# Optimization experiments

Measured on AMD Instinct MI355X. Metric: run time of the kernel, lower is better.

## Reference

```python
import jax, jax.numpy as jnp
import numpy as np

# Static diagonal offsets of the SparseDIA matrix (eqx static field).
OFFSETS = (-128, -64, -8, -1, 0, 1, 8, 64, 128)
N = 8192   # matrix dimension (diags.shape[1])
M = 4096   # number of dense columns in `other`


def setup_inputs() -> dict:
    key = jax.random.key(0)
    k1, k2 = jax.random.split(key)
    diags = jax.random.normal(k1, (len(OFFSETS), N), dtype=jnp.float32)
    other = jax.random.normal(k2, (N, M), dtype=jnp.float32)
    return {"diags": diags, "other": other}


def reference(diags, other):
    """SparseDIA._matmul_dense(left_matmul=True): out = A_dia @ other.

    For each static offset k, rows [top:bottom] of the output accumulate
    diag[start:end] (the valid part of the stored diagonal) times the
    matching rows of `other`. Offsets are Python ints, so all slices are
    static and jit-compatible.
    """
    n = other.shape[0]
    out = jnp.zeros_like(other)
    for k, offset in enumerate(OFFSETS):
        start = max(0, offset)
        end = min(n, n + offset)
        top = max(0, -offset)
        bottom = top + (end - start)
        out = out.at[top:bottom, :].add(
            diags[k, start:end, None] * other[start:end, :]
        )
    return out
```

## Files before the change

### kernel.cpp

```cpp
#include <hip/hip_runtime.h>


#define DIA_N   8192
#define DIA_M   4096
#define M4      (DIA_M / 4)
#define CB      8
#define BR      128
#define HALO    128
#define RING    512
#define NB      16
#define GROUP   (BR * NB)
#define THREADS 1024
#define NWAVES  (THREADS / 64)

typedef float f4 __attribute__((ext_vector_type(4)));
typedef __attribute__((address_space(3))) unsigned int       lds_uint;
typedef const __attribute__((address_space(1))) unsigned int glb_uint;

__global__ __launch_bounds__(THREADS, 8) void sparse_dia_kernel(
    const float* __restrict__ diags,
    const float* __restrict__ other,
    float* __restrict__ out)
{
    constexpr int OFF[9] = {-128, -64, -8, -1, 0, 1, 8, 64, 128};

    __shared__ f4    ring[RING][CB];
    __shared__ float dlds[2][9 * BR];

    const int tid  = threadIdx.x;
    const int gr0  = blockIdx.y * GROUP;
    const int cb4  = blockIdx.x * CB;

    const int wave = tid >> 6;
    const int lane = tid & 63;
    const int lrow = lane >> 3;
    const int lcol = lane & 7;
    const int scol = lcol ^ lrow;

    auto stage_ring = [&](int slot0, int q0, int ninst) {
#pragma unroll
        for (int s = 0; s < 3; ++s) {
            if (s >= ninst) break;
            const int inst = wave * ninst + s;
            int q = q0 + inst * 8 + lrow;
            q = (q < 0) ? 0 : (q >= DIA_N ? DIA_N - 1 : q);
            const float* src = other + ((size_t)q * DIA_M + (size_t)(cb4 + scol) * 4);
            __builtin_amdgcn_global_load_lds(
                (glb_uint*)src,
                (lds_uint*)&ring[slot0 + inst * 8][0],
                16, 0, 0);
        }
    };

    auto stage_diag = [&](int buf, int t) {
        const int bs = gr0 + t * BR;
        for (int f = tid; f < 9 * BR; f += THREADS) {
            const int k  = f >> 7;
            const int i  = f & (BR - 1);
            const int q  = bs + i + OFF[k];
            const int qc = (q < 0) ? 0 : (q >= DIA_N ? DIA_N - 1 : q);
            float v = diags[k * DIA_N + qc];
            v = ((unsigned)q < (unsigned)DIA_N) ? v : 0.f;
            dlds[buf][f] = v;
        }
    };

    f4* __restrict__ out4 = (f4*)out;

    stage_ring(0, gr0 - HALO, 3);
    stage_diag(0, 0);
    __syncthreads();

    const int c = tid & 7;
    const int i = tid >> 3;

    for (int t = 0; t < NB; ++t) {
        if (t + 1 < NB) {
            const int u = (BR + 2 * HALO) + t * BR;
            stage_ring(u & (RING - 1), gr0 - HALO + u, 1);
            stage_diag((t + 1) & 1, t + 1);
        }

        const int buf  = t & 1;
        const int base = (HALO + t * BR) & (RING - 1);

        float dk[9];
#pragma unroll
        for (int k = 0; k < 9; ++k) dk[k] = dlds[buf][k * BR + i];

        f4 a = (f4){0.f, 0.f, 0.f, 0.f};
#pragma unroll
        for (int k = 0; k < 9; ++k) {
            const int slot = (base + i + OFF[k]) & (RING - 1);
            a += dk[k] * ring[slot][c ^ (slot & 7)];
        }

        out4[(size_t)(gr0 + t * BR + i) * M4 + cb4 + c] = a;

        __syncthreads();
    }
}

extern "C" void kernel_launch(void* const* d_in, const int* in_sizes, int n_in,
                              void* d_out, int out_size, void* d_ws, size_t ws_size,
                              hipStream_t stream) {
    const float* diags = (const float*)d_in[0];
    const float* other = (const float*)d_in[1];
    float* out         = (float*)d_out;

    dim3 block(THREADS, 1, 1);
    dim3 grid(M4 / CB, DIA_N / GROUP, 1);
    sparse_dia_kernel<<<grid, block, 0, stream>>>(diags, other, out);
}
```

Baseline: 244.4 us.

## Pipeline ring staging with manual vmcnt waits and register-prefetched diagonals

Halves the block to 512 threads with 64-row tiles. Diagonal coefficients are now loaded straight from global memory into registers two tiles ahead, replacing the shared-memory double buffer. Each step uses explicit s_waitcnt vmcnt counts and raw s_barrier instead of __syncthreads, so the async LDS loads for later tiles stay in flight while the current tile is computed and stored. This relies on exact counts of outstanding vector-memory ops, which is fragile, and the smaller tiles double the number of barrier steps.

```diff
diff --git a/kernel.cpp b/kernel.cpp
--- a/kernel.cpp
+++ b/kernel.cpp
@@ -5,27 +5,25 @@
 #define DIA_M   4096
 #define M4      (DIA_M / 4)
 #define CB      8
-#define BR      128
+#define BR      64
 #define HALO    128
 #define RING    512
-#define NB      16
+#define NB      32
 #define GROUP   (BR * NB)
-#define THREADS 1024
-#define NWAVES  (THREADS / 64)
+#define THREADS 512
 
 typedef float f4 __attribute__((ext_vector_type(4)));
 typedef __attribute__((address_space(3))) unsigned int       lds_uint;
 typedef const __attribute__((address_space(1))) unsigned int glb_uint;
 
-__global__ __launch_bounds__(THREADS, 8) void sparse_dia_kernel(
+__global__ __launch_bounds__(THREADS, 4) void sparse_dia_kernel(
     const float* __restrict__ diags,
     const float* __restrict__ other,
     float* __restrict__ out)
 {
     constexpr int OFF[9] = {-128, -64, -8, -1, 0, 1, 8, 64, 128};
 
-    __shared__ f4    ring[RING][CB];
-    __shared__ float dlds[2][9 * BR];
+    __shared__ f4 ring[RING][CB];
 
     const int tid  = threadIdx.x;
     const int gr0  = blockIdx.y * GROUP;
@@ -37,68 +35,81 @@
     const int lcol = lane & 7;
     const int scol = lcol ^ lrow;
 
-    auto stage_ring = [&](int slot0, int q0, int ninst) {
+    const int c = tid & 7;
+    const int i = tid >> 3;
+
+    f4* __restrict__ out4 = (f4*)out;
+
+    auto gll8 = [&](int slot0, int q0) {
+        int q = q0 + lrow;
+        q = (q < 0) ? 0 : (q >= DIA_N ? DIA_N - 1 : q);
+        const float* src = other + ((size_t)q * DIA_M + (size_t)(cb4 + scol) * 4);
+        __builtin_amdgcn_global_load_lds((glb_uint*)src,
+            (lds_uint*)&ring[slot0][0], 16, 0, 0);
+    };
+
+    auto load_diag = [&](int t, float (&dk)[9]) {
+        const int b = gr0 + t * BR + i;
+        if (gr0 + t * BR - HALO >= 0 && gr0 + t * BR + (BR - 1) + HALO < DIA_N) {
 #pragma unroll
-        for (int s = 0; s < 3; ++s) {
-            if (s >= ninst) break;
-            const int inst = wave * ninst + s;
-            int q = q0 + inst * 8 + lrow;
-            q = (q < 0) ? 0 : (q >= DIA_N ? DIA_N - 1 : q);
-            const float* src = other + ((size_t)q * DIA_M + (size_t)(cb4 + scol) * 4);
-            __builtin_amdgcn_global_load_lds(
-                (glb_uint*)src,
-                (lds_uint*)&ring[slot0 + inst * 8][0],
-                16, 0, 0);
+            for (int k = 0; k < 9; ++k)
+                dk[k] = diags[k * DIA_N + b + OFF[k]];
+        } else {
+#pragma unroll
+            for (int k = 0; k < 9; ++k) {
+                const int q  = b + OFF[k];
+                const int qc = (q < 0) ? 0 : (q >= DIA_N ? DIA_N - 1 : q);
+                const float v = diags[k * DIA_N + qc];
+                dk[k] = ((unsigned)q < (unsigned)DIA_N) ? v : 0.f;
+            }
         }
     };
 
-    auto stage_diag = [&](int buf, int t) {
-        const int bs = gr0 + t * BR;
-        for (int f = tid; f < 9 * BR; f += THREADS) {
-            const int k  = f >> 7;
-            const int i  = f & (BR - 1);
-            const int q  = bs + i + OFF[k];
-            const int qc = (q < 0) ? 0 : (q >= DIA_N ? DIA_N - 1 : q);
-            float v = diags[k * DIA_N + qc];
-            v = ((unsigned)q < (unsigned)DIA_N) ? v : 0.f;
-            dlds[buf][f] = v;
-        }
-    };
-
-    f4* __restrict__ out4 = (f4*)out;
-
-    stage_ring(0, gr0 - HALO, 3);
-    stage_diag(0, 0);
-    __syncthreads();
-
-    const int c = tid & 7;
-    const int i = tid >> 3;
-
-    for (int t = 0; t < NB; ++t) {
-        if (t + 1 < NB) {
-            const int u = (BR + 2 * HALO) + t * BR;
-            stage_ring(u & (RING - 1), gr0 - HALO + u, 1);
-            stage_diag((t + 1) & 1, t + 1);
-        }
-
-        const int buf  = t & 1;
-        const int base = (HALO + t * BR) & (RING - 1);
-
-        float dk[9];
-#pragma unroll
-        for (int k = 0; k < 9; ++k) dk[k] = dlds[buf][k * BR + i];
-
+    auto compute_store = [&](int t, const float (&dk)[9]) {
+        const int L0 = t * BR + HALO + i;
         f4 a = (f4){0.f, 0.f, 0.f, 0.f};
 #pragma unroll
         for (int k = 0; k < 9; ++k) {
-            const int slot = (base + i + OFF[k]) & (RING - 1);
-            a += dk[k] * ring[slot][c ^ (slot & 7)];
+            const int s = (L0 + OFF[k]) & (RING - 1);
+            a += dk[k] * ring[s][c ^ (s & 7)];
         }
+        out4[(size_t)(gr0 + t * BR + i) * M4 + cb4 + c] = a;
+    };
 
-        out4[(size_t)(gr0 + t * BR + i) * M4 + cb4 + c] = a;
+    float dkA[9], dkB[9];
 
-        __syncthreads();
+#pragma unroll
+    for (int s = 0; s < 5; ++s) {
+        const int inst = wave * 5 + s;
+        gll8(inst * 8, gr0 - HALO + inst * 8);
     }
+    gll8(320 + wave * 8, gr0 - HALO + 320 + wave * 8);
+    load_diag(0, dkA);
+    load_diag(1, dkB);
+    asm volatile("s_waitcnt vmcnt(0)" ::: "memory");
+    __builtin_amdgcn_s_barrier();
+    __builtin_amdgcn_sched_barrier(0);
+
+    auto body = [&](int t, float (&dk)[9]) {
+        const int Lc = t * BR + 384;
+        gll8((Lc & (RING - 1)) + wave * 8, gr0 - HALO + Lc + wave * 8);
+        compute_store(t, dk);
+        load_diag(t + 2, dk);
+        asm volatile("s_waitcnt vmcnt(11)" ::: "memory");
+        __builtin_amdgcn_s_barrier();
+        __builtin_amdgcn_sched_barrier(0);
+    };
+
+    for (int t = 0; t < NB - 2; t += 2) {
+        body(t,     dkA);
+        body(t + 1, dkB);
+    }
+
+    compute_store(NB - 2, dkA);
+    asm volatile("s_waitcnt vmcnt(1)" ::: "memory");
+    __builtin_amdgcn_s_barrier();
+    __builtin_amdgcn_sched_barrier(0);
+    compute_store(NB - 1, dkB);
 }
 
 extern "C" void kernel_launch(void* const* d_in, const int* in_sizes, int n_in,
```

Result: no change. 247.9 us (+1.4%).
